# Performance work log

Measured on AMD Instinct MI355X. Metric: run time of the kernel, lower is better.

## Reference

```python
import jax, jax.numpy as jnp
import numpy as np

B, C, K, D = 16, 128, 128, 256
EPS = 1e-5  # torch BatchNorm1d default eps


def _bn(x, gamma, beta):
    # torch BatchNorm1d training-mode on (N, ch, L): normalize each channel over (N, L)
    mean = x.mean(axis=(0, 2), keepdims=True)
    var = x.var(axis=(0, 2), keepdims=True)  # biased, matches torch normalization
    return (x - mean) / jnp.sqrt(var + EPS) * gamma[None, :, None] + beta[None, :, None]


def setup_inputs() -> dict:
    key = jax.random.key(0)
    ks = jax.random.split(key, 6)
    q = jax.random.normal(ks[0], (B, C, D), jnp.float32)
    kc = jax.random.normal(ks[1], (B, K, D), jnp.float32)
    W0 = jax.random.normal(ks[2], (D, D), jnp.float32) / np.sqrt(D)
    W1 = jax.random.normal(ks[3], (D, D), jnp.float32) / np.sqrt(D)
    cmask = jax.random.randint(ks[4], (B, C), 0, 2, jnp.int32)
    kmask = jax.random.randint(ks[5], (B, K), 0, 2, jnp.int32)
    klen = jnp.maximum(kmask.sum(axis=1), 1).astype(jnp.int32)
    return {
        "query_candidates_repr": q,
        "key_candidates": kc,
        "W0": W0,
        "W1": W1,
        "bn0_gamma": jnp.ones((C,), jnp.float32),
        "bn0_beta": jnp.zeros((C,), jnp.float32),
        "bn1_gamma": jnp.ones((K,), jnp.float32),
        "bn1_beta": jnp.zeros((K,), jnp.float32),
        "query_candidate_mask": cmask,
        "key_candidate_mask": kmask,
        "key_candidate_len": klen,
    }


def reference(query_candidates_repr, key_candidates, W0, W1,
              bn0_gamma, bn0_beta, bn1_gamma, bn1_beta,
              query_candidate_mask, key_candidate_mask, key_candidate_len):
    # gated_attention branch (att_type != 'softmax'), activate = tanh
    g0 = _bn(query_candidates_repr @ W0.T, bn0_gamma, bn0_beta)  # (B,C,D)
    g1 = _bn(key_candidates @ W1.T, bn1_gamma, bn1_beta)          # (B,K,D)
    # (B,C,K,D) gate product
    attention_weight = jax.nn.sigmoid(g1)[:, None, :, :] * jax.nn.sigmoid(g0)[:, :, None, :]
    attention_res = key_candidates[:, None, :, :] * attention_weight  # (B,C,K,D)
    mask = (query_candidate_mask[:, :, None] * key_candidate_mask[:, None, :]).astype(jnp.float32)
    attention_res_masked = attention_res * mask[..., None]
    attention_vector = attention_res_masked.sum(axis=2) / key_candidate_len[:, None, None].astype(jnp.float32)
    output_res = jnp.tanh(attention_vector)  # (B,C,D)
    return output_res, attention_res_masked, attention_weight.mean(axis=-1)
```

## Files before the change

kernel.cpp:

```cpp
#include <hip/hip_runtime.h>


#define NB 16
#define NC 128
#define NK 128
#define ND 256

typedef float f4v __attribute__((ext_vector_type(4)));

__global__ __launch_bounds__(256) void k_gemm(const float* __restrict__ q,
                                              const float* __restrict__ kc,
                                              const float* __restrict__ W0,
                                              const float* __restrict__ W1,
                                              float* __restrict__ Y) {
    __shared__ float As[16][64];
    __shared__ float Bs[16][64];
    const int m0 = blockIdx.x * 64;
    const int d0 = blockIdx.y * 64;
    const int t  = threadIdx.x;
    const float* A = (m0 < 2048) ? (q + (size_t)m0 * ND) : (kc + (size_t)(m0 - 2048) * ND);
    const float* W = (m0 < 2048) ? W0 : W1;
    const int ml = t >> 2;
    const int jl = (t & 3) * 4;
    const int ty = t >> 4;
    const int tx = t & 15;

    float acc[4][4] = {};
    for (int j0 = 0; j0 < 256; j0 += 16) {
        float4 a = *(const float4*)(A + ml * ND + j0 + jl);
        float4 b = *(const float4*)(W + (d0 + ml) * ND + j0 + jl);
        As[jl + 0][ml] = a.x; As[jl + 1][ml] = a.y; As[jl + 2][ml] = a.z; As[jl + 3][ml] = a.w;
        Bs[jl + 0][ml] = b.x; Bs[jl + 1][ml] = b.y; Bs[jl + 2][ml] = b.z; Bs[jl + 3][ml] = b.w;
        __syncthreads();
#pragma unroll
        for (int jj = 0; jj < 16; ++jj) {
            float4 av = *(const float4*)&As[jj][ty * 4];
            float4 bv = *(const float4*)&Bs[jj][tx * 4];
            acc[0][0] += av.x * bv.x; acc[0][1] += av.x * bv.y; acc[0][2] += av.x * bv.z; acc[0][3] += av.x * bv.w;
            acc[1][0] += av.y * bv.x; acc[1][1] += av.y * bv.y; acc[1][2] += av.y * bv.z; acc[1][3] += av.y * bv.w;
            acc[2][0] += av.z * bv.x; acc[2][1] += av.z * bv.y; acc[2][2] += av.z * bv.z; acc[2][3] += av.z * bv.w;
            acc[3][0] += av.w * bv.x; acc[3][1] += av.w * bv.y; acc[3][2] += av.w * bv.z; acc[3][3] += av.w * bv.w;
        }
        __syncthreads();
    }
#pragma unroll
    for (int i = 0; i < 4; ++i) {
        float4 o = make_float4(acc[i][0], acc[i][1], acc[i][2], acc[i][3]);
        *(float4*)(Y + (size_t)(m0 + ty * 4 + i) * ND + d0 + tx * 4) = o;
    }
}

__global__ __launch_bounds__(256) void k_stats(const float* __restrict__ Y,
                                               const float* __restrict__ g0, const float* __restrict__ b0,
                                               const float* __restrict__ g1, const float* __restrict__ b1,
                                               float* __restrict__ sc, float* __restrict__ sh) {
    const int ch = blockIdx.x;
    const int t  = threadIdx.x;
    const int rbase = (ch < 128) ? ch : (2048 + (ch - 128));
    float s = 0.f, s2 = 0.f;
#pragma unroll
    for (int b = 0; b < NB; ++b) {
        float v = Y[(size_t)(rbase + b * 128) * ND + t];
        s += v; s2 += v * v;
    }
#pragma unroll
    for (int off = 32; off > 0; off >>= 1) {
        s  += __shfl_down(s,  off, 64);
        s2 += __shfl_down(s2, off, 64);
    }
    __shared__ float r1[4], r2[4];
    const int w = t >> 6;
    if ((t & 63) == 0) { r1[w] = s; r2[w] = s2; }
    __syncthreads();
    if (t == 0) {
        s  = r1[0] + r1[1] + r1[2] + r1[3];
        s2 = r2[0] + r2[1] + r2[2] + r2[3];
        float mean = s * (1.f / 4096.f);
        float var  = s2 * (1.f / 4096.f) - mean * mean;
        float rstd = rsqrtf(var + 1e-5f);
        float g  = (ch < 128) ? g0[ch] : g1[ch - 128];
        float be = (ch < 128) ? b0[ch] : b1[ch - 128];
        sc[ch] = g * rstd;
        sh[ch] = be - mean * g * rstd;
    }
}

__global__ __launch_bounds__(256) void k_apply(float* __restrict__ Y,
                                               const float* __restrict__ sc, const float* __restrict__ sh) {
    const int m = blockIdx.x;
    const int t = threadIdx.x;
    const size_t idx = (size_t)m * ND + t;
    float x = Y[idx];
    const int ch = (m < 2048) ? (m & 127) : (128 + (m & 127));
    float g = x * sc[ch] + sh[ch];
    Y[idx] = 1.f / (1.f + __expf(-g));
}

__global__ __launch_bounds__(256) void k_out2(const float* __restrict__ Y,
                                              float* __restrict__ out2) {
    __shared__ float As[16][64];
    __shared__ float Bs[16][64];
    const int b  = blockIdx.z;
    const int c0 = blockIdx.x * 64;
    const int k0 = blockIdx.y * 64;
    const int t  = threadIdx.x;
    const float* A = Y + (size_t)(b * 128 + c0) * ND;
    const float* W = Y + (size_t)(2048 + b * 128 + k0) * ND;
    const int ml = t >> 2;
    const int jl = (t & 3) * 4;
    const int ty = t >> 4;
    const int tx = t & 15;

    float acc[4][4] = {};
    for (int j0 = 0; j0 < 256; j0 += 16) {
        float4 a = *(const float4*)(A + ml * ND + j0 + jl);
        float4 bv_ = *(const float4*)(W + ml * ND + j0 + jl);
        As[jl + 0][ml] = a.x; As[jl + 1][ml] = a.y; As[jl + 2][ml] = a.z; As[jl + 3][ml] = a.w;
        Bs[jl + 0][ml] = bv_.x; Bs[jl + 1][ml] = bv_.y; Bs[jl + 2][ml] = bv_.z; Bs[jl + 3][ml] = bv_.w;
        __syncthreads();
#pragma unroll
        for (int jj = 0; jj < 16; ++jj) {
            float4 av = *(const float4*)&As[jj][ty * 4];
            float4 bv = *(const float4*)&Bs[jj][tx * 4];
            acc[0][0] += av.x * bv.x; acc[0][1] += av.x * bv.y; acc[0][2] += av.x * bv.z; acc[0][3] += av.x * bv.w;
            acc[1][0] += av.y * bv.x; acc[1][1] += av.y * bv.y; acc[1][2] += av.y * bv.z; acc[1][3] += av.y * bv.w;
            acc[2][0] += av.z * bv.x; acc[2][1] += av.z * bv.y; acc[2][2] += av.z * bv.z; acc[2][3] += av.z * bv.w;
            acc[3][0] += av.w * bv.x; acc[3][1] += av.w * bv.y; acc[3][2] += av.w * bv.z; acc[3][3] += av.w * bv.w;
        }
        __syncthreads();
    }
    const float scale = 1.f / 256.f;
#pragma unroll
    for (int i = 0; i < 4; ++i) {
        float4 o = make_float4(acc[i][0] * scale, acc[i][1] * scale, acc[i][2] * scale, acc[i][3] * scale);
        *(float4*)(out2 + ((size_t)(b * 128 + c0 + ty * 4 + i)) * 128 + k0 + tx * 4) = o;
    }
}

__global__ __launch_bounds__(256) void k_u(float* __restrict__ Y,
                                           const float* __restrict__ kc,
                                           const int* __restrict__ kmask) {
    const int r = blockIdx.x;
    const int t = threadIdx.x;
    const size_t idx = (size_t)(2048 + r) * ND + t;
    const float km = (float)kmask[r];
    Y[idx] = km * kc[(size_t)r * ND + t] * Y[idx];
}

__global__ __launch_bounds__(256) void k_t(const float* __restrict__ Y,
                                           float* __restrict__ tvec) {
    const int b = blockIdx.x;
    const int t = threadIdx.x;
    const float* u = Y + (size_t)(2048 + b * 128) * ND;
    float s0 = 0.f, s1 = 0.f, s2 = 0.f, s3 = 0.f;
#pragma unroll 8
    for (int k = 0; k < 128; k += 4) {
        s0 += u[(size_t)(k + 0) * ND + t];
        s1 += u[(size_t)(k + 1) * ND + t];
        s2 += u[(size_t)(k + 2) * ND + t];
        s3 += u[(size_t)(k + 3) * ND + t];
    }
    tvec[b * ND + t] = (s0 + s1) + (s2 + s3);
}

__global__ __launch_bounds__(256) void k_big2(const float* __restrict__ Y,
                                              const float* __restrict__ tvec,
                                              const int* __restrict__ cmask,
                                              const int* __restrict__ klen,
                                              float* __restrict__ out0,
                                              float* __restrict__ out1) {
    const int bc = blockIdx.x;
    const int b  = bc >> 7;
    const int t  = threadIdx.x;
    const int f  = t & 63;
    const int g  = t >> 6;

    float4 s0v = *(const float4*)(Y + (size_t)bc * ND + f * 4);
    const bool cm = cmask[bc] != 0;
    float4 v0 = cm ? s0v : make_float4(0.f, 0.f, 0.f, 0.f);

    const float* up = Y + (size_t)(2048 + b * 128 + g) * ND + f * 4;
    float*       op = out1 + (size_t)bc * 128 * ND + (size_t)g * ND + f * 4;

#pragma unroll 4
    for (int k0 = 0; k0 < 32; ++k0) {
        float4 uv = *(const float4*)up;
        float4 o = make_float4(v0.x * uv.x, v0.y * uv.y, v0.z * uv.z, v0.w * uv.w);
        __builtin_nontemporal_store(*(const f4v*)&o, (f4v*)op);
        up += 4 * ND;
        op += 4 * ND;
    }

    if (g == 0) {
        float4 tv = *(const float4*)(tvec + b * ND + f * 4);
        const float inv = 1.f / (float)klen[b];
        float4 o0 = make_float4(tanhf(v0.x * tv.x * inv), tanhf(v0.y * tv.y * inv),
                                tanhf(v0.z * tv.z * inv), tanhf(v0.w * tv.w * inv));
        *(float4*)(out0 + (size_t)bc * ND + f * 4) = o0;
    }
}

extern "C" void kernel_launch(void* const* d_in, const int* in_sizes, int n_in,
                              void* d_out, int out_size, void* d_ws, size_t ws_size,
                              hipStream_t stream) {
    const float* q     = (const float*)d_in[0];
    const float* kc    = (const float*)d_in[1];
    const float* W0    = (const float*)d_in[2];
    const float* W1    = (const float*)d_in[3];
    const float* g0    = (const float*)d_in[4];
    const float* b0    = (const float*)d_in[5];
    const float* g1    = (const float*)d_in[6];
    const float* b1    = (const float*)d_in[7];
    const int*   cmask = (const int*)d_in[8];
    const int*   kmask = (const int*)d_in[9];
    const int*   klen  = (const int*)d_in[10];

    float* ws = (float*)d_ws;
    float* Y  = ws;
    float* sc = ws + 1048576;
    float* sh = ws + 1048832;
    float* tv = ws + 1049088;

    float* o    = (float*)d_out;
    float* out0 = o;
    float* out1 = o + 524288;
    float* out2 = o + 67633152;

    k_gemm <<<dim3(64, 4),    256, 0, stream>>>(q, kc, W0, W1, Y);
    k_stats<<<256,            256, 0, stream>>>(Y, g0, b0, g1, b1, sc, sh);
    k_apply<<<4096,           256, 0, stream>>>(Y, sc, sh);
    k_out2 <<<dim3(2, 2, 16), 256, 0, stream>>>(Y, out2);
    k_u    <<<2048,           256, 0, stream>>>(Y, kc, kmask);
    k_t    <<<16,             256, 0, stream>>>(Y, tv);
    k_big2 <<<2048,           256, 0, stream>>>(Y, tv, cmask, klen, out0, out1);
}
```

Measured before the change: 335.4 us.

## Fuse BN stats/apply/sigmoid with key reduction and merge tail kernels

Merges the BN statistics, normalization and sigmoid into one kernel that keeps each channel's values in registers and accumulates the masked key sum with atomics. The out2 GEMM, out0 tanh and the large out1 product are folded into one launch split by block index. Kernel launches drop from seven to three, removing several intermediate passes over Y. In exchange out1 now recomputes kc*mask per element instead of reading a precomputed product, and drops the nontemporal store hint. Atomics also make the tvec summation order nondeterministic.

```diff
diff --git a/kernel.cpp b/kernel.cpp
--- a/kernel.cpp
+++ b/kernel.cpp
@@ -6,13 +6,15 @@
 #define NK 128
 #define ND 256
 
-typedef float f4v __attribute__((ext_vector_type(4)));
-
 __global__ __launch_bounds__(256) void k_gemm(const float* __restrict__ q,
                                               const float* __restrict__ kc,
                                               const float* __restrict__ W0,
                                               const float* __restrict__ W1,
-                                              float* __restrict__ Y) {
+                                              float* __restrict__ Y,
+                                              float* __restrict__ tvec) {
+    if (blockIdx.x == 0 && blockIdx.y == 0) {
+        for (int i = threadIdx.x; i < NB * ND; i += 256) tvec[i] = 0.f;
+    }
     __shared__ float As[16][64];
     __shared__ float Bs[16][64];
     const int m0 = blockIdx.x * 64;
@@ -50,18 +52,21 @@
     }
 }
 
-__global__ __launch_bounds__(256) void k_stats(const float* __restrict__ Y,
-                                               const float* __restrict__ g0, const float* __restrict__ b0,
-                                               const float* __restrict__ g1, const float* __restrict__ b1,
-                                               float* __restrict__ sc, float* __restrict__ sh) {
+__global__ __launch_bounds__(256) void k_sau(float* __restrict__ Y,
+                                             const float* __restrict__ kc,
+                                             const float* __restrict__ g0, const float* __restrict__ b0,
+                                             const float* __restrict__ g1, const float* __restrict__ b1,
+                                             const int* __restrict__ kmask,
+                                             float* __restrict__ tvec) {
     const int ch = blockIdx.x;
     const int t  = threadIdx.x;
     const int rbase = (ch < 128) ? ch : (2048 + (ch - 128));
+    float v[NB];
     float s = 0.f, s2 = 0.f;
 #pragma unroll
     for (int b = 0; b < NB; ++b) {
-        float v = Y[(size_t)(rbase + b * 128) * ND + t];
-        s += v; s2 += v * v;
+        v[b] = Y[(size_t)(rbase + b * 128) * ND + t];
+        s += v[b]; s2 += v[b] * v[b];
     }
 #pragma unroll
     for (int off = 32; off > 0; off >>= 1) {
@@ -69,6 +74,7 @@
         s2 += __shfl_down(s2, off, 64);
     }
     __shared__ float r1[4], r2[4];
+    __shared__ float bsc, bsh;
     const int w = t >> 6;
     if ((t & 63) == 0) { r1[w] = s; r2[w] = s2; }
     __syncthreads();
@@ -80,123 +86,119 @@
         float rstd = rsqrtf(var + 1e-5f);
         float g  = (ch < 128) ? g0[ch] : g1[ch - 128];
         float be = (ch < 128) ? b0[ch] : b1[ch - 128];
-        sc[ch] = g * rstd;
-        sh[ch] = be - mean * g * rstd;
-    }
-}
-
-__global__ __launch_bounds__(256) void k_apply(float* __restrict__ Y,
-                                               const float* __restrict__ sc, const float* __restrict__ sh) {
-    const int m = blockIdx.x;
-    const int t = threadIdx.x;
-    const size_t idx = (size_t)m * ND + t;
-    float x = Y[idx];
-    const int ch = (m < 2048) ? (m & 127) : (128 + (m & 127));
-    float g = x * sc[ch] + sh[ch];
-    Y[idx] = 1.f / (1.f + __expf(-g));
-}
-
-__global__ __launch_bounds__(256) void k_out2(const float* __restrict__ Y,
+        bsc = g * rstd;
+        bsh = be - mean * g * rstd;
+    }
+    __syncthreads();
+    const float sc = bsc, sh = bsh;
+    if (ch < 128) {
+#pragma unroll
+        for (int b = 0; b < NB; ++b) {
+            float sig = 1.f / (1.f + __expf(-(v[b] * sc + sh)));
+            Y[(size_t)(rbase + b * 128) * ND + t] = sig;
+        }
+    } else {
+        const int k = ch - 128;
+#pragma unroll
+        for (int b = 0; b < NB; ++b) {
+            float sig = 1.f / (1.f + __expf(-(v[b] * sc + sh)));
+            Y[(size_t)(rbase + b * 128) * ND + t] = sig;
+            if (kmask[b * 128 + k] != 0) {
+                float u = kc[(size_t)(b * 128 + k) * ND + t] * sig;
+                atomicAdd(&tvec[b * ND + t], u);
+            }
+        }
+    }
+}
+
+__global__ __launch_bounds__(256) void k_tail(const float* __restrict__ Y,
+                                              const float* __restrict__ kc,
+                                              const int* __restrict__ cmask,
+                                              const int* __restrict__ kmask,
+                                              const int* __restrict__ klen,
+                                              const float* __restrict__ tvec,
+                                              float* __restrict__ out0,
+                                              float* __restrict__ out1,
                                               float* __restrict__ out2) {
     __shared__ float As[16][64];
     __shared__ float Bs[16][64];
-    const int b  = blockIdx.z;
-    const int c0 = blockIdx.x * 64;
-    const int k0 = blockIdx.y * 64;
-    const int t  = threadIdx.x;
-    const float* A = Y + (size_t)(b * 128 + c0) * ND;
-    const float* W = Y + (size_t)(2048 + b * 128 + k0) * ND;
-    const int ml = t >> 2;
-    const int jl = (t & 3) * 4;
-    const int ty = t >> 4;
-    const int tx = t & 15;
-
-    float acc[4][4] = {};
-    for (int j0 = 0; j0 < 256; j0 += 16) {
-        float4 a = *(const float4*)(A + ml * ND + j0 + jl);
-        float4 bv_ = *(const float4*)(W + ml * ND + j0 + jl);
-        As[jl + 0][ml] = a.x; As[jl + 1][ml] = a.y; As[jl + 2][ml] = a.z; As[jl + 3][ml] = a.w;
-        Bs[jl + 0][ml] = bv_.x; Bs[jl + 1][ml] = bv_.y; Bs[jl + 2][ml] = bv_.z; Bs[jl + 3][ml] = bv_.w;
-        __syncthreads();
-#pragma unroll
-        for (int jj = 0; jj < 16; ++jj) {
-            float4 av = *(const float4*)&As[jj][ty * 4];
-            float4 bv = *(const float4*)&Bs[jj][tx * 4];
-            acc[0][0] += av.x * bv.x; acc[0][1] += av.x * bv.y; acc[0][2] += av.x * bv.z; acc[0][3] += av.x * bv.w;
-            acc[1][0] += av.y * bv.x; acc[1][1] += av.y * bv.y; acc[1][2] += av.y * bv.z; acc[1][3] += av.y * bv.w;
-            acc[2][0] += av.z * bv.x; acc[2][1] += av.z * bv.y; acc[2][2] += av.z * bv.z; acc[2][3] += av.z * bv.w;
-            acc[3][0] += av.w * bv.x; acc[3][1] += av.w * bv.y; acc[3][2] += av.w * bv.z; acc[3][3] += av.w * bv.w;
-        }
-        __syncthreads();
-    }
-    const float scale = 1.f / 256.f;
-#pragma unroll
-    for (int i = 0; i < 4; ++i) {
-        float4 o = make_float4(acc[i][0] * scale, acc[i][1] * scale, acc[i][2] * scale, acc[i][3] * scale);
-        *(float4*)(out2 + ((size_t)(b * 128 + c0 + ty * 4 + i)) * 128 + k0 + tx * 4) = o;
-    }
-}
-
-__global__ __launch_bounds__(256) void k_u(float* __restrict__ Y,
-                                           const float* __restrict__ kc,
-                                           const int* __restrict__ kmask) {
-    const int r = blockIdx.x;
-    const int t = threadIdx.x;
-    const size_t idx = (size_t)(2048 + r) * ND + t;
-    const float km = (float)kmask[r];
-    Y[idx] = km * kc[(size_t)r * ND + t] * Y[idx];
-}
-
-__global__ __launch_bounds__(256) void k_t(const float* __restrict__ Y,
-                                           float* __restrict__ tvec) {
-    const int b = blockIdx.x;
-    const int t = threadIdx.x;
-    const float* u = Y + (size_t)(2048 + b * 128) * ND;
-    float s0 = 0.f, s1 = 0.f, s2 = 0.f, s3 = 0.f;
-#pragma unroll 8
-    for (int k = 0; k < 128; k += 4) {
-        s0 += u[(size_t)(k + 0) * ND + t];
-        s1 += u[(size_t)(k + 1) * ND + t];
-        s2 += u[(size_t)(k + 2) * ND + t];
-        s3 += u[(size_t)(k + 3) * ND + t];
-    }
-    tvec[b * ND + t] = (s0 + s1) + (s2 + s3);
-}
-
-__global__ __launch_bounds__(256) void k_big2(const float* __restrict__ Y,
-                                              const float* __restrict__ tvec,
-                                              const int* __restrict__ cmask,
-                                              const int* __restrict__ klen,
-                                              float* __restrict__ out0,
-                                              float* __restrict__ out1) {
-    const int bc = blockIdx.x;
-    const int b  = bc >> 7;
-    const int t  = threadIdx.x;
-    const int f  = t & 63;
-    const int g  = t >> 6;
-
-    float4 s0v = *(const float4*)(Y + (size_t)bc * ND + f * 4);
-    const bool cm = cmask[bc] != 0;
-    float4 v0 = cm ? s0v : make_float4(0.f, 0.f, 0.f, 0.f);
-
-    const float* up = Y + (size_t)(2048 + b * 128 + g) * ND + f * 4;
-    float*       op = out1 + (size_t)bc * 128 * ND + (size_t)g * ND + f * 4;
+    const int bid = blockIdx.x;
+    const int t   = threadIdx.x;
+
+    if (bid < 64) {
+        const int b  = bid >> 2;
+        const int c0 = ((bid >> 1) & 1) * 64;
+        const int k0 = (bid & 1) * 64;
+        const float* A = Y + (size_t)(b * 128 + c0) * ND;
+        const float* W = Y + (size_t)(2048 + b * 128 + k0) * ND;
+        const int ml = t >> 2;
+        const int jl = (t & 3) * 4;
+        const int ty = t >> 4;
+        const int tx = t & 15;
+        float acc[4][4] = {};
+        for (int j0 = 0; j0 < 256; j0 += 16) {
+            float4 a  = *(const float4*)(A + ml * ND + j0 + jl);
+            float4 bb = *(const float4*)(W + ml * ND + j0 + jl);
+            As[jl + 0][ml] = a.x;  As[jl + 1][ml] = a.y;  As[jl + 2][ml] = a.z;  As[jl + 3][ml] = a.w;
+            Bs[jl + 0][ml] = bb.x; Bs[jl + 1][ml] = bb.y; Bs[jl + 2][ml] = bb.z; Bs[jl + 3][ml] = bb.w;
+            __syncthreads();
+#pragma unroll
+            for (int jj = 0; jj < 16; ++jj) {
+                float4 av = *(const float4*)&As[jj][ty * 4];
+                float4 bv = *(const float4*)&Bs[jj][tx * 4];
+                acc[0][0] += av.x * bv.x; acc[0][1] += av.x * bv.y; acc[0][2] += av.x * bv.z; acc[0][3] += av.x * bv.w;
+                acc[1][0] += av.y * bv.x; acc[1][1] += av.y * bv.y; acc[1][2] += av.y * bv.z; acc[1][3] += av.y * bv.w;
+                acc[2][0] += av.z * bv.x; acc[2][1] += av.z * bv.y; acc[2][2] += av.z * bv.z; acc[2][3] += av.z * bv.w;
+                acc[3][0] += av.w * bv.x; acc[3][1] += av.w * bv.y; acc[3][2] += av.w * bv.z; acc[3][3] += av.w * bv.w;
+            }
+            __syncthreads();
+        }
+        const float scale = 1.f / 256.f;
+#pragma unroll
+        for (int i = 0; i < 4; ++i) {
+            float4 o = make_float4(acc[i][0] * scale, acc[i][1] * scale, acc[i][2] * scale, acc[i][3] * scale);
+            *(float4*)(out2 + ((size_t)(b * 128 + c0 + ty * 4 + i)) * 128 + k0 + tx * 4) = o;
+        }
+    } else if (bid < 320) {
+        const int local = bid - 64;
+        const int b  = local >> 4;
+        const int c0 = (local & 15) * 8;
+        const float tv  = tvec[b * ND + t];
+        const float inv = 1.f / (float)klen[b];
+#pragma unroll
+        for (int ci = 0; ci < 8; ++ci) {
+            const int bc = b * 128 + c0 + ci;
+            const float cm = (cmask[bc] != 0) ? 1.f : 0.f;
+            const float s0 = Y[(size_t)bc * ND + t];
+            out0[(size_t)bc * ND + t] = tanhf(cm * s0 * tv * inv);
+        }
+    } else {
+        const int bc = bid - 320;
+        const int b  = bc >> 7;
+        const int f  = t & 63;
+        const int g  = t >> 6;
+        float4 s0v = *(const float4*)(Y + (size_t)bc * ND + f * 4);
+        const bool cm = cmask[bc] != 0;
+        float4 v0 = cm ? s0v : make_float4(0.f, 0.f, 0.f, 0.f);
+
+        const float* s1p = Y  + (size_t)(2048 + b * 128 + g) * ND + f * 4;
+        const float* kcp = kc + (size_t)(b * 128 + g) * ND + f * 4;
+        const int*   kmb = kmask + b * 128;
+        float*       op  = out1 + (size_t)bc * 128 * ND + (size_t)g * ND + f * 4;
 
 #pragma unroll 4
-    for (int k0 = 0; k0 < 32; ++k0) {
-        float4 uv = *(const float4*)up;
-        float4 o = make_float4(v0.x * uv.x, v0.y * uv.y, v0.z * uv.z, v0.w * uv.w);
-        __builtin_nontemporal_store(*(const f4v*)&o, (f4v*)op);
-        up += 4 * ND;
-        op += 4 * ND;
-    }
-
-    if (g == 0) {
-        float4 tv = *(const float4*)(tvec + b * ND + f * 4);
-        const float inv = 1.f / (float)klen[b];
-        float4 o0 = make_float4(tanhf(v0.x * tv.x * inv), tanhf(v0.y * tv.y * inv),
-                                tanhf(v0.z * tv.z * inv), tanhf(v0.w * tv.w * inv));
-        *(float4*)(out0 + (size_t)bc * ND + f * 4) = o0;
+        for (int k0 = 0; k0 < 32; ++k0) {
+            const int k = k0 * 4 + g;
+            const float km = (float)kmb[k];
+            float4 s1v = *(const float4*)s1p;
+            float4 kcv = *(const float4*)kcp;
+            float4 o = make_float4(v0.x * km * kcv.x * s1v.x,
+                                   v0.y * km * kcv.y * s1v.y,
+                                   v0.z * km * kcv.z * s1v.z,
+                                   v0.w * km * kcv.w * s1v.w);
+            *(float4*)op = o;
+            s1p += 4 * ND; kcp += 4 * ND; op += 4 * ND;
+        }
     }
 }
 
@@ -217,20 +219,14 @@
 
     float* ws = (float*)d_ws;
     float* Y  = ws;
-    float* sc = ws + 1048576;
-    float* sh = ws + 1048832;
-    float* tv = ws + 1049088;
+    float* tv = ws + 1048576;
 
     float* o    = (float*)d_out;
     float* out0 = o;
     float* out1 = o + 524288;
     float* out2 = o + 67633152;
 
-    k_gemm <<<dim3(64, 4),    256, 0, stream>>>(q, kc, W0, W1, Y);
-    k_stats<<<256,            256, 0, stream>>>(Y, g0, b0, g1, b1, sc, sh);
-    k_apply<<<4096,           256, 0, stream>>>(Y, sc, sh);
-    k_out2 <<<dim3(2, 2, 16), 256, 0, stream>>>(Y, out2);
-    k_u    <<<2048,           256, 0, stream>>>(Y, kc, kmask);
-    k_t    <<<16,             256, 0, stream>>>(Y, tv);
-    k_big2 <<<2048,           256, 0, stream>>>(Y, tv, cmask, klen, out0, out1);
-}
+    k_gemm<<<dim3(64, 4), 256, 0, stream>>>(q, kc, W0, W1, Y, tv);
+    k_sau <<<256,         256, 0, stream>>>(Y, kc, g0, b0, g1, b1, kmask, tv);
+    k_tail<<<2368,        256, 0, stream>>>(Y, kc, cmask, kmask, klen, tv, out0, out1, out2);
+}
```

Result: faster. 324.4 us (-3.3%).
